# Performance work log

Measured on AMD Instinct MI355X. Metric: run time of the kernel, lower is better.

## Reference

```python
import jax, jax.numpy as jnp
import numpy as np

N, E, B = 24000, 96000, 1200
NPG = N // B  # nodes per graph

def _lin(k, fi, fo):
    s = 1.0 / np.sqrt(fi)
    return jax.random.uniform(k, (fi, fo), jnp.float32, -s, s)

def setup_inputs():
    key = jax.random.key(0)
    ks = jax.random.split(key, 32)
    x = jax.random.normal(ks[0], (N, 9), jnp.float32)
    edge_attr = jax.random.normal(ks[1], (E, 4), jnp.float32)
    src = jax.random.randint(ks[2], (E,), 0, N)
    # destination node within the same graph as the source (block-diagonal adjacency)
    dst = (src // NPG) * NPG + jax.random.randint(ks[3], (E,), 0, NPG)
    edge_index = jnp.stack([src, dst]).astype(jnp.int32)
    batch = (jnp.arange(N) // NPG).astype(jnp.int32)
    fp_batch = jax.random.normal(ks[4], (B, 2048), jnp.float32)
    p = dict(
        Wq1=_lin(ks[5], 9, 512), bq1=jnp.zeros(512, jnp.float32),
        Wk1=_lin(ks[6], 9, 512), bk1=jnp.zeros(512, jnp.float32),
        Wv1=_lin(ks[7], 9, 512), bv1=jnp.zeros(512, jnp.float32),
        We1=_lin(ks[8], 4, 512),
        Ws1=_lin(ks[9], 9, 512), bs1=jnp.zeros(512, jnp.float32),
        Wq2=_lin(ks[10], 512, 1024), bq2=jnp.zeros(1024, jnp.float32),
        Wk2=_lin(ks[11], 512, 1024), bk2=jnp.zeros(1024, jnp.float32),
        Wv2=_lin(ks[12], 512, 1024), bv2=jnp.zeros(1024, jnp.float32),
        We2=_lin(ks[13], 4, 1024),
        Ws2=_lin(ks[14], 512, 1024), bs2=jnp.zeros(1024, jnp.float32),
        Wfp=_lin(ks[15], 2048, 256), bfp=jnp.zeros(256, jnp.float32),
        Wfin=_lin(ks[16], 1280, 1024), bfin=jnp.zeros(1024, jnp.float32),
    )
    return dict(x=x, edge_index=edge_index, edge_attr=edge_attr, batch=batch, fp_batch=fp_batch, **p)

def _tconv(x, src, dst, ea, Wq, bq, Wk, bk, Wv, bv, We, Ws, bs, H, C):
    """PyG TransformerConv: concat=True, beta=False, root_weight=True."""
    n = x.shape[0]
    q = (x @ Wq + bq).reshape(n, H, C)
    k = (x @ Wk + bk).reshape(n, H, C)
    v = (x @ Wv + bv).reshape(n, H, C)
    e = (ea @ We).reshape(-1, H, C)            # lin_edge has no bias
    ke = k[src] + e                            # [E,H,C]
    alpha = jnp.einsum('ehc,ehc->eh', q[dst], ke) / jnp.sqrt(jnp.float32(C))
    # scatter-softmax over incoming edges of each target node
    amax = jax.ops.segment_max(alpha, dst, num_segments=n)
    amax = jnp.where(jnp.isfinite(amax), amax, 0.0)  # nodes with no in-edges
    ex = jnp.exp(alpha - amax[dst])
    den = jax.ops.segment_sum(ex, dst, num_segments=n)[dst] + 1e-16
    msg = (v[src] + e) * (ex / den)[:, :, None]
    out = jax.ops.segment_sum(msg, dst, num_segments=n).reshape(n, H * C)
    return out + x @ Ws + bs                   # root/skip connection

def reference(x, edge_index, edge_attr, batch, fp_batch, Wq1, bq1, Wk1, bk1, Wv1, bv1, We1, Ws1, bs1, Wq2, bq2, Wk2, bk2, Wv2, bv2, We2, Ws2, bs2, Wfp, bfp, Wfin, bfin):
    src, dst = edge_index[0], edge_index[1]
    h = jax.nn.relu(_tconv(x, src, dst, edge_attr, Wq1, bq1, Wk1, bk1, Wv1, bv1, We1, Ws1, bs1, 4, 128))
    h = _tconv(h, src, dst, edge_attr, Wq2, bq2, Wk2, bk2, Wv2, bv2, We2, Ws2, bs2, 4, 256)
    cnt = jax.ops.segment_sum(jnp.ones((h.shape[0],), h.dtype), batch, num_segments=B)
    g = jax.ops.segment_sum(h, batch, num_segments=B) / cnt[:, None]  # global_mean_pool
    fp = fp_batch @ Wfp + bfp
    return jnp.concatenate([g, fp], axis=-1) @ Wfin + bfin
```

## Files before the change

### kernel.cpp

```cpp
#include <hip/hip_runtime.h>
#include <cstdint>
#include <cstddef>

static constexpr int NN = 24000;
static constexpr int NE = 96000;
static constexpr int NB = 1200;
static constexpr int NPG = 20;
static constexpr int MPAD = 24064;

typedef __attribute__((ext_vector_type(8))) short bfv8;
typedef __attribute__((ext_vector_type(4))) float fv4;

__device__ __forceinline__ unsigned f2ord(float f){
  unsigned u = __float_as_uint(f);
  return (u & 0x80000000u) ? ~u : (u | 0x80000000u);
}
__device__ __forceinline__ float ord2f(unsigned u){
  return (u & 0x80000000u) ? __uint_as_float(u & 0x7FFFFFFFu)
                           : __uint_as_float(~u);
}
__device__ __forceinline__ unsigned short f2bf(float f){
  unsigned u = __float_as_uint(f);
  u += 0x7FFFu + ((u >> 16) & 1u);
  return (unsigned short)(u >> 16);
}
__device__ __forceinline__ float bf2f(unsigned short s){
  return __uint_as_float(((unsigned)s) << 16);
}

__global__ __launch_bounds__(256) void count_kernel(const int* __restrict__ dst,
                                                    unsigned* __restrict__ deg)
{
  int e = blockIdx.x*256 + threadIdx.x;
  if (e < NE) atomicAdd(&deg[dst[e]], 1u);
}

__global__ __launch_bounds__(1024) void scan_kernel(const unsigned* __restrict__ deg,
                                                    unsigned* __restrict__ rowstart)
{
  __shared__ unsigned s[1024];
  __shared__ unsigned carry_s;
  int tid = threadIdx.x;
  if (tid == 0) carry_s = 0;
  __syncthreads();
  for (int base = 0; base < NN; base += 1024){
    unsigned v = (base + tid < NN) ? deg[base + tid] : 0u;
    s[tid] = v;
    __syncthreads();
#pragma unroll
    for (int off = 1; off < 1024; off <<= 1){
      unsigned t = (tid >= off) ? s[tid - off] : 0u;
      __syncthreads();
      s[tid] += t;
      __syncthreads();
    }
    unsigned carry = carry_s;
    if (base + tid < NN) rowstart[base + tid] = carry + s[tid] - v;
    __syncthreads();
    if (tid == 0) carry_s = carry + s[1023];
    __syncthreads();
  }
  if (tid == 0) rowstart[NN] = carry_s;
}

__global__ __launch_bounds__(256) void scatter_kernel(const int* __restrict__ dst,
                                                      const unsigned* __restrict__ rowstart,
                                                      unsigned* __restrict__ cur,
                                                      int* __restrict__ eidx)
{
  int e = blockIdx.x*256 + threadIdx.x;
  if (e >= NE) return;
  int d = dst[e];
  unsigned p = rowstart[d] + atomicAdd(&cur[d], 1u);
  eidx[p] = e;
}

template<bool BA, bool BB>
__global__ __launch_bounds__(256) void node_gemm_l1_pair(
    const float* __restrict__ x,
    const float* __restrict__ Wa, const float* __restrict__ ba,
    const float* __restrict__ Wb, const float* __restrict__ bb,
    void* __restrict__ outa, void* __restrict__ outb)
{
  int t = blockIdx.x*256 + threadIdx.x;
  if (t >= NN*512) return;
  int n = t >> 9, j = t & 511;
  float xr[9];
#pragma unroll
  for (int i=0;i<9;i++) xr[i] = x[n*9+i];
  float aa=ba[j], ab=bb[j];
#pragma unroll
  for (int i=0;i<9;i++){
    float xi = xr[i];
    aa += xi*Wa[i*512+j];
    ab += xi*Wb[i*512+j];
  }
  if (BA) ((unsigned short*)outa)[t] = f2bf(aa); else ((float*)outa)[t] = aa;
  if (BB) ((unsigned short*)outb)[t] = f2bf(ab); else ((float*)outb)[t] = ab;
}

__global__ __launch_bounds__(256) void alpha_bf16_hc512(
    const unsigned short* __restrict__ q, const unsigned short* __restrict__ k,
    const float* __restrict__ ea, const float* __restrict__ We,
    const int* __restrict__ src, const int* __restrict__ dst,
    float* __restrict__ alpha, unsigned* __restrict__ amax)
{
  int wave = (blockIdx.x*256 + threadIdx.x) >> 6;
  int lane = threadIdx.x & 63;
  if (wave >= NE) return;
  int e = wave;
  int s = src[e], d = dst[e];
  float ea0=ea[e*4+0], ea1=ea[e*4+1], ea2=ea[e*4+2], ea3=ea[e*4+3];
  const float scale = 0.088388347648318447f;
  int off = lane*8;
  bfv8 qv = *reinterpret_cast<const bfv8*>(q + (size_t)d*512 + off);
  bfv8 kv = *reinterpret_cast<const bfv8*>(k + (size_t)s*512 + off);
  float part = 0.f;
#pragma unroll
  for (int j=0;j<8;j++){
    int f = off + j;
    float ef = ea0*We[f] + ea1*We[512+f] + ea2*We[1024+f] + ea3*We[1536+f];
    part += bf2f((unsigned short)qv[j]) * (bf2f((unsigned short)kv[j]) + ef);
  }
#pragma unroll
  for (int o=8; o>=1; o>>=1) part += __shfl_xor(part, o);
  if ((lane & 15) == 0){
    int h = lane >> 4;
    float a = part*scale;
    alpha[e*4+h] = a;
    atomicMax(&amax[d*4+h], f2ord(a));
  }
}

__global__ __launch_bounds__(256) void alpha_bf16_hc1024(
    const unsigned short* __restrict__ q, const unsigned short* __restrict__ k,
    const float* __restrict__ ea, const float* __restrict__ We,
    const int* __restrict__ src, const int* __restrict__ dst,
    float* __restrict__ alpha, unsigned* __restrict__ amax)
{
  int wave = (blockIdx.x*256 + threadIdx.x) >> 6;
  int lane = threadIdx.x & 63;
  if (wave >= NE) return;
  int e = wave;
  int s = src[e], d = dst[e];
  float ea0=ea[e*4+0], ea1=ea[e*4+1], ea2=ea[e*4+2], ea3=ea[e*4+3];
  const float scale = 1.0f/16.0f;
#pragma unroll
  for (int p=0;p<2;p++){
    int off = p*512 + lane*8;
    bfv8 qv = *reinterpret_cast<const bfv8*>(q + (size_t)d*1024 + off);
    bfv8 kv = *reinterpret_cast<const bfv8*>(k + (size_t)s*1024 + off);
    float part = 0.f;
#pragma unroll
    for (int j=0;j<8;j++){
      int f = off + j;
      float ef = ea0*We[f] + ea1*We[1024+f] + ea2*We[2048+f] + ea3*We[3072+f];
      part += bf2f((unsigned short)qv[j]) * (bf2f((unsigned short)kv[j]) + ef);
    }
#pragma unroll
    for (int o=16; o>=1; o>>=1) part += __shfl_xor(part, o);
    if ((lane & 31) == 0){
      int h = p*2 + (lane>>5);
      float a = part*scale;
      alpha[e*4+h] = a;
      atomicMax(&amax[d*4+h], f2ord(a));
    }
  }
}

__global__ __launch_bounds__(256) void ex_kernel(
    float* __restrict__ alpha, const unsigned* __restrict__ amax,
    const int* __restrict__ dst, float* __restrict__ den)
{
  int t = blockIdx.x*256 + threadIdx.x;
  if (t >= NE*4) return;
  int e = t>>2, h = t&3;
  int d = dst[e];
  float m = ord2f(amax[d*4+h]);
  float v = __expf(alpha[t]-m);
  alpha[t] = v;
  unsafeAtomicAdd(&den[d*4+h], v);
}

__global__ __launch_bounds__(256) void gather512_kernel(
    const unsigned short* __restrict__ v, const float* __restrict__ ea,
    const float* __restrict__ We,
    const int* __restrict__ src,
    const unsigned* __restrict__ rowstart, const int* __restrict__ eidx,
    const float* __restrict__ exw, const float* __restrict__ den,
    const unsigned short* __restrict__ accin, unsigned short* __restrict__ hb)
{
  int n = blockIdx.x;
  int tid = threadIdx.x;
  int h = tid >> 6;
  int f2 = tid*2;
  unsigned p0 = rowstart[n], p1 = rowstart[n+1];
  float2 W0 = *reinterpret_cast<const float2*>(We + 0*512 + f2);
  float2 W1 = *reinterpret_cast<const float2*>(We + 1*512 + f2);
  float2 W2 = *reinterpret_cast<const float2*>(We + 2*512 + f2);
  float2 W3 = *reinterpret_cast<const float2*>(We + 3*512 + f2);
  float rdn = 1.0f / (den[n*4+h] + 1e-16f);
  ushort2 a0 = *reinterpret_cast<const ushort2*>(accin + (size_t)n*512 + f2);
  float2 s = make_float2(bf2f(a0.x), bf2f(a0.y));
  for (unsigned p = p0; p < p1; ++p){
    int e  = eidx[p];
    float w = exw[e*4+h] * rdn;
    float4 eav = *reinterpret_cast<const float4*>(ea + (size_t)e*4);
    ushort2 vv = *reinterpret_cast<const ushort2*>(v + (size_t)src[e]*512 + f2);
    float efx = eav.x*W0.x + eav.y*W1.x + eav.z*W2.x + eav.w*W3.x;
    float efy = eav.x*W0.y + eav.y*W1.y + eav.z*W2.y + eav.w*W3.y;
    s.x += w*(bf2f(vv.x) + efx);
    s.y += w*(bf2f(vv.y) + efy);
  }
  ushort2 o;
  o.x = f2bf(fmaxf(s.x, 0.0f));
  o.y = f2bf(fmaxf(s.y, 0.0f));
  *reinterpret_cast<ushort2*>(hb + (size_t)n*512 + f2) = o;
}

__global__ __launch_bounds__(256) void gather1024_kernel(
    const unsigned short* __restrict__ v, const float* __restrict__ ea,
    const float* __restrict__ We,
    const int* __restrict__ src,
    const unsigned* __restrict__ rowstart, const int* __restrict__ eidx,
    const float* __restrict__ exw, const float* __restrict__ den,
    unsigned short* __restrict__ acc)
{
  int n = blockIdx.x;
  int tid = threadIdx.x;
  int h = tid >> 6;
  int f4 = tid*4;
  unsigned p0 = rowstart[n], p1 = rowstart[n+1];
  float4 W0 = *reinterpret_cast<const float4*>(We + 0*1024 + f4);
  float4 W1 = *reinterpret_cast<const float4*>(We + 1*1024 + f4);
  float4 W2 = *reinterpret_cast<const float4*>(We + 2*1024 + f4);
  float4 W3 = *reinterpret_cast<const float4*>(We + 3*1024 + f4);
  float rdn = 1.0f / (den[n*4+h] + 1e-16f);
  ushort4 a0 = *reinterpret_cast<const ushort4*>(acc + (size_t)n*1024 + f4);
  float4 s = make_float4(bf2f(a0.x), bf2f(a0.y), bf2f(a0.z), bf2f(a0.w));
  for (unsigned p = p0; p < p1; ++p){
    int e  = eidx[p];
    float w = exw[e*4+h] * rdn;
    float4 eav = *reinterpret_cast<const float4*>(ea + (size_t)e*4);
    ushort4 vv = *reinterpret_cast<const ushort4*>(v + (size_t)src[e]*1024 + f4);
    s.x += w*(bf2f(vv.x) + eav.x*W0.x + eav.y*W1.x + eav.z*W2.x + eav.w*W3.x);
    s.y += w*(bf2f(vv.y) + eav.x*W0.y + eav.y*W1.y + eav.z*W2.y + eav.w*W3.y);
    s.z += w*(bf2f(vv.z) + eav.x*W0.z + eav.y*W1.z + eav.z*W2.z + eav.w*W3.z);
    s.w += w*(bf2f(vv.w) + eav.x*W0.w + eav.y*W1.w + eav.z*W2.w + eav.w*W3.w);
  }
  ushort4 o;
  o.x = f2bf(s.x); o.y = f2bf(s.y); o.z = f2bf(s.z); o.w = f2bf(s.w);
  *reinterpret_cast<ushort4*>(acc + (size_t)n*1024 + f4) = o;
}

__global__ __launch_bounds__(256) void cvt_wt_kernel(const float* __restrict__ W,
                                                     unsigned short* __restrict__ Wt)
{
  int t = blockIdx.x*256 + threadIdx.x;
  if (t >= 1024*512) return;
  int n = t >> 9, k = t & 511;
  Wt[t] = f2bf(W[k*1024 + n]);
}

template<bool BOUT>
__global__ __launch_bounds__(256) void gemm_bf16_mfma(
    const unsigned short* __restrict__ A,
    const unsigned short* __restrict__ B,
    const float* __restrict__ bias,
    void* __restrict__ Cout, int M)
{
  constexpr int K = 512, N = 1024;
  __shared__ unsigned short As[128*32];
  __shared__ unsigned short Bs[128*32];
  int tid  = threadIdx.x;
  int wid  = tid >> 6, lane = tid & 63;
  int wr   = wid >> 1, wc = wid & 1;
  int bm   = blockIdx.y * 128, bn = blockIdx.x * 128;
  int l15  = lane & 15, kg = lane >> 4;

  int r0 = (wid*2+0)*16 + (lane>>2);
  int r1 = (wid*2+1)*16 + (lane>>2);
  int s0 = lane & 3;
  int kc0 = s0 ^ ((r0>>1)&3);
  int kc1 = s0 ^ ((r1>>1)&3);
  unsigned short* ldsA0 = As + (wid*2+0)*512;
  unsigned short* ldsA1 = As + (wid*2+1)*512;
  unsigned short* ldsB0 = Bs + (wid*2+0)*512;
  unsigned short* ldsB1 = Bs + (wid*2+1)*512;

  fv4 acc[4][4];
#pragma unroll
  for (int m=0;m<4;m++)
#pragma unroll
    for (int n=0;n<4;n++) acc[m][n] = (fv4){0.f,0.f,0.f,0.f};

  for (int k0 = 0; k0 < K; k0 += 32){
    __syncthreads();
    __builtin_amdgcn_global_load_lds(
        (const __attribute__((address_space(1))) void*)(A + (size_t)(bm+r0)*K + k0 + kc0*8),
        (__attribute__((address_space(3))) void*)ldsA0, 16, 0, 0);
    __builtin_amdgcn_global_load_lds(
        (const __attribute__((address_space(1))) void*)(A + (size_t)(bm+r1)*K + k0 + kc1*8),
        (__attribute__((address_space(3))) void*)ldsA1, 16, 0, 0);
    __builtin_amdgcn_global_load_lds(
        (const __attribute__((address_space(1))) void*)(B + (size_t)(bn+r0)*K + k0 + kc0*8),
        (__attribute__((address_space(3))) void*)ldsB0, 16, 0, 0);
    __builtin_amdgcn_global_load_lds(
        (const __attribute__((address_space(1))) void*)(B + (size_t)(bn+r1)*K + k0 + kc1*8),
        (__attribute__((address_space(3))) void*)ldsB1, 16, 0, 0);
    __syncthreads();
    bfv8 af[4], bfr[4];
#pragma unroll
    for (int m=0;m<4;m++){
      int r  = wr*64 + m*16 + l15;
      int sl = kg ^ ((r>>1)&3);
      af[m] = *reinterpret_cast<const bfv8*>(reinterpret_cast<char*>(As) + r*64 + sl*16);
    }
#pragma unroll
    for (int n=0;n<4;n++){
      int r  = wc*64 + n*16 + l15;
      int sl = kg ^ ((r>>1)&3);
      bfr[n] = *reinterpret_cast<const bfv8*>(reinterpret_cast<char*>(Bs) + r*64 + sl*16);
    }
#pragma unroll
    for (int m=0;m<4;m++)
#pragma unroll
      for (int n=0;n<4;n++)
        acc[m][n] = __builtin_amdgcn_mfma_f32_16x16x32_bf16(af[m], bfr[n], acc[m][n], 0, 0, 0);
  }
#pragma unroll
  for (int m=0;m<4;m++){
#pragma unroll
    for (int n=0;n<4;n++){
      int col = bn + wc*64 + n*16 + l15;
      float bcol = bias[col];
#pragma unroll
      for (int r=0;r<4;r++){
        int row = bm + wr*64 + m*16 + (lane>>4)*4 + r;
        if (row < M){
          float val = acc[m][n][r] + bcol;
          if (BOUT) ((unsigned short*)Cout)[(size_t)row*N + col] = f2bf(val);
          else      ((float*)Cout)[(size_t)row*N + col] = val;
        }
      }
    }
  }
}

__global__ __launch_bounds__(256) void sgemm_partial(
    const float* __restrict__ A, const float* __restrict__ W,
    float* __restrict__ P, int M, int N, int K, int kchunk, int zoff)
{
  __shared__ float As[32][68];
  __shared__ __align__(16) float Bs[32][64];
  int tid = threadIdx.x;
  int bm = blockIdx.y*64, bn = blockIdx.x*64;
  int kbeg = blockIdx.z*kchunk;
  int kend = min(kbeg + kchunk, K);
  float* Pz = P + (size_t)(zoff + blockIdx.z)*M*N;
  int ty = tid >> 4, tx = tid & 15;
  float acc[4][4] = {};
  for (int k0 = kbeg; k0 < kend; k0 += 32){
#pragma unroll
    for (int i=0;i<2;i++){
      int lin = tid + i*256;
      int r = lin >> 3;
      int kq = (lin & 7) * 4;
      float4 av = make_float4(0.f,0.f,0.f,0.f);
      int row = bm + r;
      if (row < M) av = *reinterpret_cast<const float4*>(A + (size_t)row*K + k0 + kq);
      As[kq+0][r]=av.x; As[kq+1][r]=av.y; As[kq+2][r]=av.z; As[kq+3][r]=av.w;
    }
#pragma unroll
    for (int i=0;i<2;i++){
      int lin = tid + i*256;
      int kr = lin >> 4;
      int c4 = (lin & 15) * 4;
      float4 wv = *reinterpret_cast<const float4*>(W + (size_t)(k0+kr)*N + bn + c4);
      *reinterpret_cast<float4*>(&Bs[kr][c4]) = wv;
    }
    __syncthreads();
#pragma unroll
    for (int kk=0;kk<32;kk++){
      float a[4], b[4];
#pragma unroll
      for (int i=0;i<4;i++) a[i] = As[kk][ty*4+i];
#pragma unroll
      for (int j=0;j<4;j++) b[j] = Bs[kk][tx*4+j];
#pragma unroll
      for (int i=0;i<4;i++)
#pragma unroll
        for (int j=0;j<4;j++) acc[i][j] += a[i]*b[j];
    }
    __syncthreads();
  }
#pragma unroll
  for (int i=0;i<4;i++){
    int row = bm + ty*4 + i;
    if (row >= M) break;
#pragma unroll
    for (int j=0;j<4;j++)
      Pz[(size_t)row*N + bn + tx*4 + j] = acc[i][j];
  }
}

__global__ __launch_bounds__(256) void reduce_add_kernel(
    const float* __restrict__ P, const float* __restrict__ bias,
    float* __restrict__ O, int total, int nz, int nmask)
{
  int t = blockIdx.x*256 + threadIdx.x;
  if (t >= total) return;
  float s = bias[t & nmask];
  for (int z = 0; z < nz; ++z) s += P[(size_t)z*total + t];
  O[t] = s;
}

__global__ __launch_bounds__(256) void pool_kernel(const unsigned short* __restrict__ h2,
                                                   float* __restrict__ g)
{
  int t = blockIdx.x*256 + threadIdx.x;
  if (t >= NB*256) return;
  int b = t >> 8, f4 = (t & 255) * 4;
  float4 s = make_float4(0.f,0.f,0.f,0.f);
#pragma unroll
  for (int i=0;i<NPG;i++){
    ushort4 v = *reinterpret_cast<const ushort4*>(h2 + (size_t)(b*NPG+i)*1024 + f4);
    s.x += bf2f(v.x); s.y += bf2f(v.y); s.z += bf2f(v.z); s.w += bf2f(v.w);
  }
  s.x *= (1.0f/NPG); s.y *= (1.0f/NPG); s.z *= (1.0f/NPG); s.w *= (1.0f/NPG);
  *reinterpret_cast<float4*>(g + (size_t)b*1024 + f4) = s;
}

extern "C" void kernel_launch(void* const* d_in, const int* in_sizes, int n_in,
                              void* d_out, int out_size, void* d_ws, size_t ws_size,
                              hipStream_t stream)
{
  const float* x    = (const float*)d_in[0];
  const int*   ei   = (const int*)d_in[1];
  const float* ea   = (const float*)d_in[2];
  const float* fpb  = (const float*)d_in[4];
  const float* Wq1  = (const float*)d_in[5];  const float* bq1 = (const float*)d_in[6];
  const float* Wk1  = (const float*)d_in[7];  const float* bk1 = (const float*)d_in[8];
  const float* Wv1  = (const float*)d_in[9];  const float* bv1 = (const float*)d_in[10];
  const float* We1  = (const float*)d_in[11];
  const float* Ws1  = (const float*)d_in[12]; const float* bs1 = (const float*)d_in[13];
  const float* Wq2  = (const float*)d_in[14]; const float* bq2 = (const float*)d_in[15];
  const float* Wk2  = (const float*)d_in[16]; const float* bk2 = (const float*)d_in[17];
  const float* Wv2  = (const float*)d_in[18]; const float* bv2 = (const float*)d_in[19];
  const float* We2  = (const float*)d_in[20];
  const float* Ws2  = (const float*)d_in[21]; const float* bs2 = (const float*)d_in[22];
  const float* Wfp  = (const float*)d_in[23]; const float* bfp = (const float*)d_in[24];
  const float* Wfin = (const float*)d_in[25]; const float* bfin= (const float*)d_in[26];
  const int* src = ei;
  const int* dst = ei + NE;
  float* out = (float*)d_out;

  const size_t F512  = (size_t)NN*512;
  const size_t F1024 = (size_t)NN*1024;
  float* base = (float*)d_ws;
  float* C_a = base;
  float* C_b = base + F1024;
  float* H   = base + 2*F1024;
  unsigned short* q1b = (unsigned short*)C_a;
  unsigned short* v1b = (unsigned short*)C_a;
  unsigned short* k1b = (unsigned short*)H;
  unsigned short* s1b = (unsigned short*)H;
  unsigned short* hb  = (unsigned short*)C_a + F1024;
  unsigned short* q2b = (unsigned short*)C_a;
  unsigned short* k2b = (unsigned short*)C_b;
  unsigned short* v2b = (unsigned short*)C_a;
  unsigned short* s2b = (unsigned short*)C_b;
  unsigned short* WtQ = (unsigned short*)H;
  unsigned short* WtK = WtQ + (size_t)1024*512;
  unsigned short* WtV = WtK + (size_t)1024*512;
  unsigned short* WtS = WtV + (size_t)1024*512;
  float* P1 = C_a;
  float* P2 = C_a + 5*(size_t)NB*1024;

  float* tail = base + 2*F1024 + F512;
  float*    alphab   = tail;
  unsigned* amax     = (unsigned*)(alphab + (size_t)NE*4);
  float*    den      = (float*)(amax + (size_t)NN*4);
  unsigned* deg      = (unsigned*)(den + (size_t)NN*4);
  unsigned* cur      = deg + NN;
  unsigned* rowstart = cur + NN;
  int*      eidx     = (int*)(rowstart + NN + 1);
  float*    g        = (float*)(eidx + NE);
  float*    fp       = g + (size_t)NB*1024;

  hipMemsetAsync(deg, 0, sizeof(unsigned)*NN, stream);
  hipMemsetAsync(cur, 0, sizeof(unsigned)*NN, stream);
  count_kernel<<<(NE+255)/256, 256, 0, stream>>>(dst, deg);
  scan_kernel<<<1, 1024, 0, stream>>>(deg, rowstart);
  scatter_kernel<<<(NE+255)/256, 256, 0, stream>>>(dst, rowstart, cur, eidx);

  hipMemsetAsync(amax, 0, sizeof(unsigned)*(size_t)NN*4, stream);
  hipMemsetAsync(den,  0, sizeof(float)*(size_t)NN*4, stream);

  node_gemm_l1_pair<true,true><<<(NN*512+255)/256, 256, 0, stream>>>(
      x, Wq1,bq1, Wk1,bk1, q1b, k1b);
  alpha_bf16_hc512<<<NE/4, 256, 0, stream>>>(q1b, k1b, ea, We1, src, dst, alphab, amax);
  ex_kernel<<<(NE*4+255)/256, 256, 0, stream>>>(alphab, amax, dst, den);
  node_gemm_l1_pair<true,true><<<(NN*512+255)/256, 256, 0, stream>>>(
      x, Wv1,bv1, Ws1,bs1, v1b, s1b);
  gather512_kernel<<<NN, 256, 0, stream>>>(v1b, ea, We1, src, rowstart, eidx,
                                           alphab, den, s1b, hb);
  hipMemsetAsync(hb + F512, 0, (size_t)(MPAD-NN)*512*sizeof(unsigned short), stream);

  cvt_wt_kernel<<<(1024*512+255)/256, 256, 0, stream>>>(Wq2, WtQ);
  cvt_wt_kernel<<<(1024*512+255)/256, 256, 0, stream>>>(Wk2, WtK);
  cvt_wt_kernel<<<(1024*512+255)/256, 256, 0, stream>>>(Wv2, WtV);
  cvt_wt_kernel<<<(1024*512+255)/256, 256, 0, stream>>>(Ws2, WtS);

  hipMemsetAsync(amax, 0, sizeof(unsigned)*(size_t)NN*4, stream);
  hipMemsetAsync(den,  0, sizeof(float)*(size_t)NN*4, stream);

  {
    dim3 grid(8, MPAD/128);
    gemm_bf16_mfma<true><<<grid, 256, 0, stream>>>(hb, WtQ, bq2, q2b, NN);
    gemm_bf16_mfma<true><<<grid, 256, 0, stream>>>(hb, WtK, bk2, k2b, NN);
  }
  alpha_bf16_hc1024<<<NE/4, 256, 0, stream>>>(q2b, k2b, ea, We2, src, dst, alphab, amax);
  ex_kernel<<<(NE*4+255)/256, 256, 0, stream>>>(alphab, amax, dst, den);
  {
    dim3 grid(8, MPAD/128);
    gemm_bf16_mfma<true><<<grid, 256, 0, stream>>>(hb, WtV, bv2, v2b, NN);
    gemm_bf16_mfma<true><<<grid, 256, 0, stream>>>(hb, WtS, bs2, s2b, NN);
  }
  gather1024_kernel<<<NN, 256, 0, stream>>>(v2b, ea, We2, src, rowstart, eidx,
                                            alphab, den, s2b);

  pool_kernel<<<(NB*256+255)/256, 256, 0, stream>>>(s2b, g);

  {
    dim3 gfp(256/64, (NB+63)/64, 8);
    sgemm_partial<<<gfp, 256, 0, stream>>>(fpb, Wfp, P2, NB, 256, 2048, 256, 0);
    reduce_add_kernel<<<(NB*256+255)/256, 256, 0, stream>>>(P2, bfp, fp, NB*256, 8, 255);
  }
  {
    dim3 g1(1024/64, (NB+63)/64, 4);
    sgemm_partial<<<g1, 256, 0, stream>>>(g, Wfin, P1, NB, 1024, 1024, 256, 0);
    dim3 g2(1024/64, (NB+63)/64, 1);
    sgemm_partial<<<g2, 256, 0, stream>>>(fp, Wfin + (size_t)1024*1024, P1, NB, 1024, 256, 256, 4);
    reduce_add_kernel<<<(NB*1024+255)/256, 256, 0, stream>>>(P1, bfin, out, NB*1024, 5, 1023);
  }
}
```

Baseline: 816.3 us.

## Fuse attention scores and segment softmax into per-destination-node CSR kernels

Replaces the per-edge alpha kernel (with atomicMax into amax), the separate exp/atomicAdd kernel and their memsets with one wave-per-destination-node kernel per layer. It walks the CSR incoming edges, computes the scores, and does max, exp, sum and normalise locally, writing final weights that the gather kernels read directly. It also factors the edge-feature term algebraically as ea·(q·We), so the per-edge We projection inside the dot product goes away. In exchange, load balance now depends on node in-degree and the softmax is done serially by one lane per head.

```diff
diff --git a/kernel.cpp b/kernel.cpp
--- a/kernel.cpp
+++ b/kernel.cpp
@@ -11,14 +11,6 @@
 typedef __attribute__((ext_vector_type(8))) short bfv8;
 typedef __attribute__((ext_vector_type(4))) float fv4;
 
-__device__ __forceinline__ unsigned f2ord(float f){
-  unsigned u = __float_as_uint(f);
-  return (u & 0x80000000u) ? ~u : (u | 0x80000000u);
-}
-__device__ __forceinline__ float ord2f(unsigned u){
-  return (u & 0x80000000u) ? __uint_as_float(u & 0x7FFFFFFFu)
-                           : __uint_as_float(~u);
-}
 __device__ __forceinline__ unsigned short f2bf(float f){
   unsigned u = __float_as_uint(f);
   u += 0x7FFFu + ((u >> 16) & 1u);
@@ -99,87 +91,151 @@
   if (BB) ((unsigned short*)outb)[t] = f2bf(ab); else ((float*)outb)[t] = ab;
 }
 
-__global__ __launch_bounds__(256) void alpha_bf16_hc512(
+__global__ __launch_bounds__(256) void alpha_fused512(
     const unsigned short* __restrict__ q, const unsigned short* __restrict__ k,
     const float* __restrict__ ea, const float* __restrict__ We,
-    const int* __restrict__ src, const int* __restrict__ dst,
-    float* __restrict__ alpha, unsigned* __restrict__ amax)
+    const int* __restrict__ src,
+    const unsigned* __restrict__ rowstart, const int* __restrict__ eidx,
+    float* __restrict__ w)
 {
   int wave = (blockIdx.x*256 + threadIdx.x) >> 6;
   int lane = threadIdx.x & 63;
-  if (wave >= NE) return;
-  int e = wave;
-  int s = src[e], d = dst[e];
-  float ea0=ea[e*4+0], ea1=ea[e*4+1], ea2=ea[e*4+2], ea3=ea[e*4+3];
+  if (wave >= NN) return;
+  int n = wave;
+  unsigned p0 = rowstart[n], p1 = rowstart[n+1];
+  if (p0 == p1) return;
   const float scale = 0.088388347648318447f;
   int off = lane*8;
-  bfv8 qv = *reinterpret_cast<const bfv8*>(q + (size_t)d*512 + off);
-  bfv8 kv = *reinterpret_cast<const bfv8*>(k + (size_t)s*512 + off);
-  float part = 0.f;
+  bfv8 qv = *reinterpret_cast<const bfv8*>(q + (size_t)n*512 + off);
+  float t0=0.f,t1=0.f,t2=0.f,t3=0.f;
 #pragma unroll
   for (int j=0;j<8;j++){
+    float qf = bf2f((unsigned short)qv[j]);
     int f = off + j;
-    float ef = ea0*We[f] + ea1*We[512+f] + ea2*We[1024+f] + ea3*We[1536+f];
-    part += bf2f((unsigned short)qv[j]) * (bf2f((unsigned short)kv[j]) + ef);
-  }
-#pragma unroll
-  for (int o=8; o>=1; o>>=1) part += __shfl_xor(part, o);
-  if ((lane & 15) == 0){
-    int h = lane >> 4;
-    float a = part*scale;
-    alpha[e*4+h] = a;
-    atomicMax(&amax[d*4+h], f2ord(a));
-  }
-}
-
-__global__ __launch_bounds__(256) void alpha_bf16_hc1024(
+    t0 += qf*We[f]; t1 += qf*We[512+f]; t2 += qf*We[1024+f]; t3 += qf*We[1536+f];
+  }
+#pragma unroll
+  for (int o=8;o>=1;o>>=1){
+    t0 += __shfl_xor(t0,o); t1 += __shfl_xor(t1,o);
+    t2 += __shfl_xor(t2,o); t3 += __shfl_xor(t3,o);
+  }
+  bool el = (lane & 15) == 0;
+  int h = lane >> 4;
+  float mx = -__builtin_inff();
+  for (unsigned pp = p0; pp < p1; ++pp){
+    int e = eidx[pp];
+    int s = src[e];
+    bfv8 kv = *reinterpret_cast<const bfv8*>(k + (size_t)s*512 + off);
+    float part = 0.f;
+#pragma unroll
+    for (int j=0;j<8;j++)
+      part += bf2f((unsigned short)qv[j]) * bf2f((unsigned short)kv[j]);
+#pragma unroll
+    for (int o=8;o>=1;o>>=1) part += __shfl_xor(part,o);
+    if (el){
+      float4 eav = *reinterpret_cast<const float4*>(ea + (size_t)e*4);
+      float a = (part + eav.x*t0 + eav.y*t1 + eav.z*t2 + eav.w*t3)*scale;
+      w[e*4+h] = a;
+      mx = fmaxf(mx, a);
+    }
+  }
+  if (el){
+    float sum = 0.f;
+    for (unsigned pp = p0; pp < p1; ++pp){
+      int e = eidx[pp];
+      float ex = __expf(w[e*4+h] - mx);
+      w[e*4+h] = ex;
+      sum += ex;
+    }
+    float r = 1.0f / (sum + 1e-16f);
+    for (unsigned pp = p0; pp < p1; ++pp){
+      int e = eidx[pp];
+      w[e*4+h] *= r;
+    }
+  }
+}
+
+__global__ __launch_bounds__(256) void alpha_fused1024(
     const unsigned short* __restrict__ q, const unsigned short* __restrict__ k,
     const float* __restrict__ ea, const float* __restrict__ We,
-    const int* __restrict__ src, const int* __restrict__ dst,
-    float* __restrict__ alpha, unsigned* __restrict__ amax)
+    const int* __restrict__ src,
+    const unsigned* __restrict__ rowstart, const int* __restrict__ eidx,
+    float* __restrict__ w)
 {
   int wave = (blockIdx.x*256 + threadIdx.x) >> 6;
   int lane = threadIdx.x & 63;
-  if (wave >= NE) return;
-  int e = wave;
-  int s = src[e], d = dst[e];
-  float ea0=ea[e*4+0], ea1=ea[e*4+1], ea2=ea[e*4+2], ea3=ea[e*4+3];
+  if (wave >= NN) return;
+  int n = wave;
+  unsigned p0 = rowstart[n], p1 = rowstart[n+1];
+  if (p0 == p1) return;
   const float scale = 1.0f/16.0f;
-#pragma unroll
-  for (int p=0;p<2;p++){
-    int off = p*512 + lane*8;
-    bfv8 qv = *reinterpret_cast<const bfv8*>(q + (size_t)d*1024 + off);
-    bfv8 kv = *reinterpret_cast<const bfv8*>(k + (size_t)s*1024 + off);
-    float part = 0.f;
+  int off = lane*8;
+  bfv8 qv0 = *reinterpret_cast<const bfv8*>(q + (size_t)n*1024 + off);
+  bfv8 qv1 = *reinterpret_cast<const bfv8*>(q + (size_t)n*1024 + 512 + off);
+  float a0=0.f,a1=0.f,a2=0.f,a3=0.f, b0=0.f,b1=0.f,b2=0.f,b3=0.f;
+#pragma unroll
+  for (int j=0;j<8;j++){
+    float q0 = bf2f((unsigned short)qv0[j]);
+    float q1 = bf2f((unsigned short)qv1[j]);
+    int f0 = off + j, f1 = 512 + off + j;
+    a0 += q0*We[f0];      a1 += q0*We[1024+f0];
+    a2 += q0*We[2048+f0]; a3 += q0*We[3072+f0];
+    b0 += q1*We[f1];      b1 += q1*We[1024+f1];
+    b2 += q1*We[2048+f1]; b3 += q1*We[3072+f1];
+  }
+#pragma unroll
+  for (int o=16;o>=1;o>>=1){
+    a0 += __shfl_xor(a0,o); a1 += __shfl_xor(a1,o);
+    a2 += __shfl_xor(a2,o); a3 += __shfl_xor(a3,o);
+    b0 += __shfl_xor(b0,o); b1 += __shfl_xor(b1,o);
+    b2 += __shfl_xor(b2,o); b3 += __shfl_xor(b3,o);
+  }
+  bool el = (lane & 31) == 0;
+  int hg = lane >> 5;
+  int h0 = hg, h1 = 2 + hg;
+  float mx0 = -__builtin_inff(), mx1 = -__builtin_inff();
+  for (unsigned pp = p0; pp < p1; ++pp){
+    int e = eidx[pp];
+    int s = src[e];
+    bfv8 kv0 = *reinterpret_cast<const bfv8*>(k + (size_t)s*1024 + off);
+    bfv8 kv1 = *reinterpret_cast<const bfv8*>(k + (size_t)s*1024 + 512 + off);
+    float p0f = 0.f, p1f = 0.f;
 #pragma unroll
     for (int j=0;j<8;j++){
-      int f = off + j;
-      float ef = ea0*We[f] + ea1*We[1024+f] + ea2*We[2048+f] + ea3*We[3072+f];
-      part += bf2f((unsigned short)qv[j]) * (bf2f((unsigned short)kv[j]) + ef);
-    }
-#pragma unroll
-    for (int o=16; o>=1; o>>=1) part += __shfl_xor(part, o);
-    if ((lane & 31) == 0){
-      int h = p*2 + (lane>>5);
-      float a = part*scale;
-      alpha[e*4+h] = a;
-      atomicMax(&amax[d*4+h], f2ord(a));
-    }
-  }
-}
-
-__global__ __launch_bounds__(256) void ex_kernel(
-    float* __restrict__ alpha, const unsigned* __restrict__ amax,
-    const int* __restrict__ dst, float* __restrict__ den)
-{
-  int t = blockIdx.x*256 + threadIdx.x;
-  if (t >= NE*4) return;
-  int e = t>>2, h = t&3;
-  int d = dst[e];
-  float m = ord2f(amax[d*4+h]);
-  float v = __expf(alpha[t]-m);
-  alpha[t] = v;
-  unsafeAtomicAdd(&den[d*4+h], v);
+      p0f += bf2f((unsigned short)qv0[j]) * bf2f((unsigned short)kv0[j]);
+      p1f += bf2f((unsigned short)qv1[j]) * bf2f((unsigned short)kv1[j]);
+    }
+#pragma unroll
+    for (int o=16;o>=1;o>>=1){
+      p0f += __shfl_xor(p0f,o);
+      p1f += __shfl_xor(p1f,o);
+    }
+    if (el){
+      float4 eav = *reinterpret_cast<const float4*>(ea + (size_t)e*4);
+      float s0 = (p0f + eav.x*a0 + eav.y*a1 + eav.z*a2 + eav.w*a3)*scale;
+      float s1 = (p1f + eav.x*b0 + eav.y*b1 + eav.z*b2 + eav.w*b3)*scale;
+      w[e*4+h0] = s0;
+      w[e*4+h1] = s1;
+      mx0 = fmaxf(mx0, s0);
+      mx1 = fmaxf(mx1, s1);
+    }
+  }
+  if (el){
+    float sum0 = 0.f, sum1 = 0.f;
+    for (unsigned pp = p0; pp < p1; ++pp){
+      int e = eidx[pp];
+      float e0 = __expf(w[e*4+h0] - mx0);
+      float e1 = __expf(w[e*4+h1] - mx1);
+      w[e*4+h0] = e0; w[e*4+h1] = e1;
+      sum0 += e0; sum1 += e1;
+    }
+    float r0 = 1.0f/(sum0 + 1e-16f), r1 = 1.0f/(sum1 + 1e-16f);
+    for (unsigned pp = p0; pp < p1; ++pp){
+      int e = eidx[pp];
+      w[e*4+h0] *= r0;
+      w[e*4+h1] *= r1;
+    }
+  }
 }
 
 __global__ __launch_bounds__(256) void gather512_kernel(
@@ -187,7 +243,7 @@
     const float* __restrict__ We,
     const int* __restrict__ src,
     const unsigned* __restrict__ rowstart, const int* __restrict__ eidx,
-    const float* __restrict__ exw, const float* __restrict__ den,
+    const float* __restrict__ wgt,
     const unsigned short* __restrict__ accin, unsigned short* __restrict__ hb)
 {
   int n = blockIdx.x;
@@ -199,12 +255,11 @@
   float2 W1 = *reinterpret_cast<const float2*>(We + 1*512 + f2);
   float2 W2 = *reinterpret_cast<const float2*>(We + 2*512 + f2);
   float2 W3 = *reinterpret_cast<const float2*>(We + 3*512 + f2);
-  float rdn = 1.0f / (den[n*4+h] + 1e-16f);
   ushort2 a0 = *reinterpret_cast<const ushort2*>(accin + (size_t)n*512 + f2);
   float2 s = make_float2(bf2f(a0.x), bf2f(a0.y));
   for (unsigned p = p0; p < p1; ++p){
     int e  = eidx[p];
-    float w = exw[e*4+h] * rdn;
+    float w = wgt[e*4+h];
     float4 eav = *reinterpret_cast<const float4*>(ea + (size_t)e*4);
     ushort2 vv = *reinterpret_cast<const ushort2*>(v + (size_t)src[e]*512 + f2);
     float efx = eav.x*W0.x + eav.y*W1.x + eav.z*W2.x + eav.w*W3.x;
@@ -223,7 +278,7 @@
     const float* __restrict__ We,
     const int* __restrict__ src,
     const unsigned* __restrict__ rowstart, const int* __restrict__ eidx,
-    const float* __restrict__ exw, const float* __restrict__ den,
+    const float* __restrict__ wgt,
     unsigned short* __restrict__ acc)
 {
   int n = blockIdx.x;
@@ -235,12 +290,11 @@
   float4 W1 = *reinterpret_cast<const float4*>(We + 1*1024 + f4);
   float4 W2 = *reinterpret_cast<const float4*>(We + 2*1024 + f4);
   float4 W3 = *reinterpret_cast<const float4*>(We + 3*1024 + f4);
-  float rdn = 1.0f / (den[n*4+h] + 1e-16f);
   ushort4 a0 = *reinterpret_cast<const ushort4*>(acc + (size_t)n*1024 + f4);
   float4 s = make_float4(bf2f(a0.x), bf2f(a0.y), bf2f(a0.z), bf2f(a0.w));
   for (unsigned p = p0; p < p1; ++p){
     int e  = eidx[p];
-    float w = exw[e*4+h] * rdn;
+    float w = wgt[e*4+h];
     float4 eav = *reinterpret_cast<const float4*>(ea + (size_t)e*4);
     ushort4 vv = *reinterpret_cast<const ushort4*>(v + (size_t)src[e]*1024 + f4);
     s.x += w*(bf2f(vv.x) + eav.x*W0.x + eav.y*W1.x + eav.z*W2.x + eav.w*W3.x);
@@ -479,9 +533,7 @@
 
   float* tail = base + 2*F1024 + F512;
   float*    alphab   = tail;
-  unsigned* amax     = (unsigned*)(alphab + (size_t)NE*4);
-  float*    den      = (float*)(amax + (size_t)NN*4);
-  unsigned* deg      = (unsigned*)(den + (size_t)NN*4);
+  unsigned* deg      = (unsigned*)(alphab + (size_t)NE*4);
   unsigned* cur      = deg + NN;
   unsigned* rowstart = cur + NN;
   int*      eidx     = (int*)(rowstart + NN + 1);
@@ -494,17 +546,14 @@
   scan_kernel<<<1, 1024, 0, stream>>>(deg, rowstart);
   scatter_kernel<<<(NE+255)/256, 256, 0, stream>>>(dst, rowstart, cur, eidx);
 
-  hipMemsetAsync(amax, 0, sizeof(unsigned)*(size_t)NN*4, stream);
-  hipMemsetAsync(den,  0, sizeof(float)*(size_t)NN*4, stream);
-
   node_gemm_l1_pair<true,true><<<(NN*512+255)/256, 256, 0, stream>>>(
       x, Wq1,bq1, Wk1,bk1, q1b, k1b);
-  alpha_bf16_hc512<<<NE/4, 256, 0, stream>>>(q1b, k1b, ea, We1, src, dst, alphab, amax);
-  ex_kernel<<<(NE*4+255)/256, 256, 0, stream>>>(alphab, amax, dst, den);
+  alpha_fused512<<<(NN*64+255)/256, 256, 0, stream>>>(
+      q1b, k1b, ea, We1, src, rowstart, eidx, alphab);
   node_gemm_l1_pair<true,true><<<(NN*512+255)/256, 256, 0, stream>>>(
       x, Wv1,bv1, Ws1,bs1, v1b, s1b);
   gather512_kernel<<<NN, 256, 0, stream>>>(v1b, ea, We1, src, rowstart, eidx,
-                                           alphab, den, s1b, hb);
+                                           alphab, s1b, hb);
   hipMemsetAsync(hb + F512, 0, (size_t)(MPAD-NN)*512*sizeof(unsigned short), stream);
 
   cvt_wt_kernel<<<(1024*512+255)/256, 256, 0, stream>>>(Wq2, WtQ);
@@ -512,23 +561,20 @@
   cvt_wt_kernel<<<(1024*512+255)/256, 256, 0, stream>>>(Wv2, WtV);
   cvt_wt_kernel<<<(1024*512+255)/256, 256, 0, stream>>>(Ws2, WtS);
 
-  hipMemsetAsync(amax, 0, sizeof(unsigned)*(size_t)NN*4, stream);
-  hipMemsetAsync(den,  0, sizeof(float)*(size_t)NN*4, stream);
-
   {
     dim3 grid(8, MPAD/128);
     gemm_bf16_mfma<true><<<grid, 256, 0, stream>>>(hb, WtQ, bq2, q2b, NN);
     gemm_bf16_mfma<true><<<grid, 256, 0, stream>>>(hb, WtK, bk2, k2b, NN);
   }
-  alpha_bf16_hc1024<<<NE/4, 256, 0, stream>>>(q2b, k2b, ea, We2, src, dst, alphab, amax);
-  ex_kernel<<<(NE*4+255)/256, 256, 0, stream>>>(alphab, amax, dst, den);
+  alpha_fused1024<<<(NN*64+255)/256, 256, 0, stream>>>(
+      q2b, k2b, ea, We2, src, rowstart, eidx, alphab);
   {
     dim3 grid(8, MPAD/128);
     gemm_bf16_mfma<true><<<grid, 256, 0, stream>>>(hb, WtV, bv2, v2b, NN);
     gemm_bf16_mfma<true><<<grid, 256, 0, stream>>>(hb, WtS, bs2, s2b, NN);
   }
   gather1024_kernel<<<NN, 256, 0, stream>>>(v2b, ea, We2, src, rowstart, eidx,
-                                            alphab, den, s2b);
+                                            alphab, s2b);
 
   pool_kernel<<<(NB*256+255)/256, 256, 0, stream>>>(s2b, g);
 
```

New measurement: 827.1 us. Within noise of the previous version (+1.3%).
